# Kernel optimization log

Measured on AMD Instinct MI355X. Metric: run time of the kernel, lower is better.

The kernel has to match this reference:

```python
import jax, jax.numpy as jnp
import numpy as np

LSTM_SIZE = 32
NUM_OPS = 64
NUM_EDGE = 128
TEMPERATURE = 5.0
TANH_CONST = 2.5


def _lstm_cell(x, h, c, W_ih, W_hh, b_ih, b_hh):
    # PyTorch gate order: i, f, g, o
    g = x @ W_ih.T + b_ih + h @ W_hh.T + b_hh  # [4*H]
    i, f, gg, o = jnp.split(g, 4)
    c2 = jax.nn.sigmoid(f) * c + jax.nn.sigmoid(i) * jnp.tanh(gg)
    h2 = jax.nn.sigmoid(o) * jnp.tanh(c2)
    return h2, c2


def setup_inputs() -> dict:
    key = jax.random.key(0)
    ks = jax.random.split(key, 12)
    H, G, O = LSTM_SIZE, 4 * LSTM_SIZE, NUM_OPS
    s = 0.1
    return {
        "input_vars": jax.random.uniform(ks[0], (1, 1, H), jnp.float32, -s, s),
        "W_ih0": jax.random.uniform(ks[1], (G, H), jnp.float32, -s, s),
        "W_hh0": jax.random.uniform(ks[2], (G, H), jnp.float32, -s, s),
        "b_ih0": jax.random.uniform(ks[3], (G,), jnp.float32, -s, s),
        "b_hh0": jax.random.uniform(ks[4], (G,), jnp.float32, -s, s),
        "W_ih1": jax.random.uniform(ks[5], (G, H), jnp.float32, -s, s),
        "W_hh1": jax.random.uniform(ks[6], (G, H), jnp.float32, -s, s),
        "b_ih1": jax.random.uniform(ks[7], (G,), jnp.float32, -s, s),
        "b_hh1": jax.random.uniform(ks[8], (G,), jnp.float32, -s, s),
        "embd": jax.random.uniform(ks[9], (O, H), jnp.float32, -s, s),
        "W_pred": jax.random.uniform(ks[10], (O, H), jnp.float32, -s, s),
        "b_pred": jax.random.uniform(ks[11], (O,), jnp.float32, -s, s),
        "num_edge": NUM_EDGE,
    }


def reference(input_vars, W_ih0, W_hh0, b_ih0, b_hh0,
              W_ih1, W_hh1, b_ih1, b_hh1,
              embd, W_pred, b_pred, num_edge):
    H = input_vars.shape[-1]
    x0 = input_vars.reshape(H)
    z = jnp.zeros((H,), input_vars.dtype)
    key0 = jax.random.key(42)

    def step(carry, _):
        key, x, h0, c0, h1, c1 = carry
        h0, c0 = _lstm_cell(x, h0, c0, W_ih0, W_hh0, b_ih0, b_hh0)
        h1, c1 = _lstm_cell(h0, h1, c1, W_ih1, W_hh1, b_ih1, b_hh1)
        logits = TANH_CONST * jnp.tanh((h1 @ W_pred.T + b_pred) / TEMPERATURE)
        key, sub = jax.random.split(key)
        idx = jax.random.categorical(sub, logits)
        logp = jax.nn.log_softmax(logits)
        lp = logp[idx]
        ent = -jnp.sum(jnp.exp(logp) * logp)
        x = embd[idx]
        return (key, x, h0, c0, h1, c1), (lp, ent, idx)

    _, (lps, ents, arch) = jax.lax.scan(step, (key0, x0, z, z, z, z), None, length=num_edge)
    return jnp.sum(lps), jnp.sum(ents), arch
```

## Files before the change

kernel.cpp:

```cpp
#include <hip/hip_runtime.h>
#include <stdint.h>

namespace {

typedef float v2f __attribute__((ext_vector_type(2)));
typedef int   v2i __attribute__((ext_vector_type(2)));

constexpr int H      = 32;
constexpr int NEDGE  = 128;
constexpr float TINY   = 1.1754943508222875e-38f;
constexpr float L2E    = 1.4426950408889634f;
constexpr float LN2    = 0.6931471805599453f;

__device__ __forceinline__ void tf_round(uint32_t& x0, uint32_t& x1, int r) {
  x0 += x1;
  x1 = (x1 << r) | (x1 >> (32 - r));
  x1 ^= x0;
}

__device__ __forceinline__ void tf2x32(uint32_t k0, uint32_t k1,
                                       uint32_t& x0, uint32_t& x1) {
  const uint32_t ks2 = k0 ^ k1 ^ 0x1BD11BDAu;
  x0 += k0; x1 += k1;
  tf_round(x0,x1,13); tf_round(x0,x1,15); tf_round(x0,x1,26); tf_round(x0,x1, 6);
  x0 += k1;  x1 += ks2 + 1u;
  tf_round(x0,x1,17); tf_round(x0,x1,29); tf_round(x0,x1,16); tf_round(x0,x1,24);
  x0 += ks2; x1 += k0 + 2u;
  tf_round(x0,x1,13); tf_round(x0,x1,15); tf_round(x0,x1,26); tf_round(x0,x1, 6);
  x0 += k0;  x1 += k1 + 3u;
  tf_round(x0,x1,17); tf_round(x0,x1,29); tf_round(x0,x1,16); tf_round(x0,x1,24);
  x0 += k1;  x1 += ks2 + 4u;
  tf_round(x0,x1,13); tf_round(x0,x1,15); tf_round(x0,x1,26); tf_round(x0,x1, 6);
  x0 += ks2; x1 += k0 + 5u;
}

__device__ __forceinline__ float fexp(float x) {
  return __builtin_amdgcn_exp2f(x * L2E);
}
__device__ __forceinline__ float flog(float x) {
  return __builtin_amdgcn_logf(x) * LN2;
}
__device__ __forceinline__ float fsigmoid(float x) {
  return __builtin_amdgcn_rcpf(1.0f + __builtin_amdgcn_exp2f(-x * L2E));
}
__device__ __forceinline__ float ftanh(float x) {
  const float ax = __builtin_fabsf(x);
  const float t  = __builtin_amdgcn_exp2f(ax * (-2.0f * L2E));
  const float r  = (1.0f - t) * __builtin_amdgcn_rcpf(1.0f + t);
  return __builtin_copysignf(r, x);
}

__device__ __forceinline__ float rdlane(float v, int i) {
  return __int_as_float(__builtin_amdgcn_readlane(__float_as_int(v), i));
}

template <int CTRL>
__device__ __forceinline__ float dppf(float v) {
  return __int_as_float(__builtin_amdgcn_update_dpp(
      __float_as_int(v), __float_as_int(v), CTRL, 0xF, 0xF, false));
}

__device__ __forceinline__ float wave_sum64(float v) {
  v += dppf<0xB1>(v);
  v += dppf<0x4E>(v);
  v += dppf<0x141>(v);
  v += dppf<0x140>(v);
  return (rdlane(v, 15) + rdlane(v, 31)) + (rdlane(v, 47) + rdlane(v, 63));
}

__device__ __forceinline__ float wave_max64(float v) {
  v = fmaxf(v, dppf<0xB1>(v));
  v = fmaxf(v, dppf<0x4E>(v));
  v = fmaxf(v, dppf<0x141>(v));
  v = fmaxf(v, dppf<0x140>(v));
  return fmaxf(fmaxf(rdlane(v, 15), rdlane(v, 31)),
               fmaxf(rdlane(v, 47), rdlane(v, 63)));
}

__device__ __forceinline__ v2f pkfma(v2f a, v2f b, v2f c) {
  return __builtin_elementwise_fma(a, b, c);
}

__device__ __forceinline__ v2f permswap_pair(float g) {
  const v2i r = __builtin_amdgcn_permlane32_swap(
      __float_as_int(g), __float_as_int(g), false, false);
  return v2f{__int_as_float(r.x), __int_as_float(r.y)};
}

__global__ __launch_bounds__(192, 1)
void ctrl_kernel(const float* __restrict__ input_vars,
                 const float* __restrict__ W_ih0, const float* __restrict__ W_hh0,
                 const float* __restrict__ b_ih0, const float* __restrict__ b_hh0,
                 const float* __restrict__ W_ih1, const float* __restrict__ W_hh1,
                 const float* __restrict__ b_ih1, const float* __restrict__ b_hh1,
                 const float* __restrict__ embd,
                 const float* __restrict__ W_pred, const float* __restrict__ b_pred,
                 float* __restrict__ out) {
  const int tid  = threadIdx.x;
  const int lane = tid & 63;
  const int wid  = tid >> 6;
  const int rB   = lane + 64;

  __shared__ float4 Wh[2][8][128];
  __shared__ __align__(16) float embd_lds[65 * H];
  __shared__ __align__(16) float gumL[NEDGE][64];
  __shared__ __align__(16) float logitL[NEDGE][64];
  __shared__ __align__(16) float archL[NEDGE];
  __shared__ int gumflag;
  __shared__ int smflag;

  if (tid == 0) { gumflag = 0; smflag = 0; }

  if (wid < 2) {
#define STAGE(MAT, SRC)                                                    \
  _Pragma("unroll")                                                        \
  for (int j = 0; j < 8; ++j) {                                            \
    const int i = (tid & 127) + 128 * j;                                   \
    const int k4 = i & 7, row = i >> 3;                                    \
    Wh[MAT][k4][row] = reinterpret_cast<const float4*>(SRC)[row * 8 + k4]; \
  }
    STAGE(0, W_hh0)
    STAGE(1, W_hh1)
#undef STAGE
  } else {
#pragma unroll
    for (int j = 0; j < 8; ++j)
      reinterpret_cast<float4*>(embd_lds)[lane + 64 * j] =
          reinterpret_cast<const float4*>(embd)[lane + 64 * j];
    if (lane < 8)
      reinterpret_cast<float4*>(&embd_lds[64 * H])[lane] =
          reinterpret_cast<const float4*>(input_vars)[lane];
  }
  __syncthreads();
  if (wid == 1) return;

  if (wid == 2) {
    uint32_t k0 = 0u, k1 = 42u;
    for (int t = 0; t < NEDGE; ++t) {
      uint32_t r0 = 0u, r1 = (uint32_t)(lane & 1);
      tf2x32(k0, k1, r0, r1);
      const uint32_t n0 = (uint32_t)__builtin_amdgcn_readlane((int)r0, 0);
      const uint32_t n1 = (uint32_t)__builtin_amdgcn_readlane((int)r1, 0);
      const uint32_t s0 = (uint32_t)__builtin_amdgcn_readlane((int)r0, 1);
      const uint32_t s1 = (uint32_t)__builtin_amdgcn_readlane((int)r1, 1);
      uint32_t x0 = 0u, x1 = (uint32_t)lane;
      tf2x32(s0, s1, x0, x1);
      const uint32_t bits = x0 ^ x1;
      k0 = n0; k1 = n1;
      float u = __uint_as_float(0x3f800000u | (bits >> 9)) - 1.0f;
      u = fmaxf(u + TINY, TINY);
      gumL[t][lane] = -flog(-flog(u));
      __threadfence_block();
      *(volatile int*)&gumflag = t + 1;
    }
    float lp_sum = 0.f, ent_sum = 0.f;
    int seen = 0;
    for (int t = 0; t < NEDGE; ++t) {
      if (seen < t + 1) {
        int v = *(volatile int*)&smflag;
        while (v < t + 1) { __builtin_amdgcn_s_sleep(2); v = *(volatile int*)&smflag; }
        seen = v;
        __threadfence_block();
      }
      const float lg  = logitL[t][lane];
      const int  idxp = (int)archL[t];
      const float e  = fexp(lg);
      const float E  = wave_sum64(e);
      const float ES = wave_sum64(e * lg);
      const float lse = flog(E);
      const float li  = logitL[t][idxp];
      lp_sum  += li - lse;
      ent_sum += lse - ES / E;
    }
    if (lane == 0) { out[0] = lp_sum; out[1] = ent_sum; }
    return;
  }

  float4 wxA0[8], wxB0[8];
  float4 wx1A[8], wx1B[8];
  float4 wp4[8];
#pragma unroll
  for (int q = 0; q < 8; ++q) {
    wxA0[q] = reinterpret_cast<const float4*>(W_ih0 + lane * H)[q];
    wxB0[q] = reinterpret_cast<const float4*>(W_ih0 + rB * H)[q];
    wx1A[q] = reinterpret_cast<const float4*>(W_ih1 + lane * H)[q];
    wx1B[q] = reinterpret_cast<const float4*>(W_ih1 + rB * H)[q];
    wp4[q]  = reinterpret_cast<const float4*>(W_pred + lane * H)[q];
  }
  const float bsum0A = b_ih0[lane] + b_hh0[lane];
  const float bsum0B = b_ih0[rB]   + b_hh0[rB];
  const float bsum1A = b_ih1[lane] + b_hh1[lane];
  const float bsum1B = b_ih1[rB]   + b_hh1[rB];
  const float bp = b_pred[lane];

  float c0 = 0.f, h0v = 0.f, c1 = 0.f, h1v = 0.f;
  v2f hoA01={0.f,0.f}, hoA23={0.f,0.f}, hoB01={0.f,0.f}, hoB23={0.f,0.f};
  v2f r1A01={0.f,0.f}, r1A23={0.f,0.f}, r1B01={0.f,0.f}, r1B23={0.f,0.f};
  float xdA, xdB;
  {
    v2f xA01={0.f,0.f}, xA23={0.f,0.f}, xB01={0.f,0.f}, xB23={0.f,0.f};
#pragma unroll
    for (int q = 0; q < 8; ++q) {
      const float4 x4 = *reinterpret_cast<const float4*>(&embd_lds[64 * H + 4 * q]);
      xA01 = pkfma(v2f{x4.x, x4.y}, v2f{wxA0[q].x, wxA0[q].y}, xA01);
      xA23 = pkfma(v2f{x4.z, x4.w}, v2f{wxA0[q].z, wxA0[q].w}, xA23);
      xB01 = pkfma(v2f{x4.x, x4.y}, v2f{wxB0[q].x, wxB0[q].y}, xB01);
      xB23 = pkfma(v2f{x4.z, x4.w}, v2f{wxB0[q].z, wxB0[q].w}, xB23);
    }
    xdA = (xA01.x + xA01.y) + (xA23.x + xA23.y);
    xdB = (xB01.x + xB01.y) + (xB23.x + xB23.y);
  }

  int gseen = 0;
  for (int t = 0; t < NEDGE; ++t) {
    if (gseen < t + 1) {
      int v = *(volatile int*)&gumflag;
      while (v < t + 1) { __builtin_amdgcn_s_sleep(2); v = *(volatile int*)&gumflag; }
      gseen = v;
      __threadfence_block();
    }
    const float gum = gumL[t][lane];

    {
      const float gA = (bsum0A + xdA)
                     + ((hoA01.x + hoA01.y) + (hoA23.x + hoA23.y));
      const float gB = (bsum0B + xdB)
                     + ((hoB01.x + hoB01.y) + (hoB23.x + hoB23.y));
      const v2f gif = permswap_pair(gA);
      const v2f ggo = permswap_pair(gB);
      c0 = fsigmoid(gif.y) * c0 + fsigmoid(gif.x) * ftanh(ggo.x);
      h0v = fsigmoid(ggo.y) * ftanh(c0);
    }

    {
#pragma unroll
      for (int q = 0; q < 8; ++q) {
        const v2f h01 = {rdlane(h0v, 4*q+0), rdlane(h0v, 4*q+1)};
        const v2f h23 = {rdlane(h0v, 4*q+2), rdlane(h0v, 4*q+3)};
        r1A01 = pkfma(h01, v2f{wx1A[q].x, wx1A[q].y}, r1A01);
        r1A23 = pkfma(h23, v2f{wx1A[q].z, wx1A[q].w}, r1A23);
        r1B01 = pkfma(h01, v2f{wx1B[q].x, wx1B[q].y}, r1B01);
        r1B23 = pkfma(h23, v2f{wx1B[q].z, wx1B[q].w}, r1B23);
      }
      const float gA1 = bsum1A + ((r1A01.x + r1A01.y) + (r1A23.x + r1A23.y));
      const float gB1 = bsum1B + ((r1B01.x + r1B01.y) + (r1B23.x + r1B23.y));
      const v2f gif1 = permswap_pair(gA1);
      const v2f ggo1 = permswap_pair(gB1);
      c1  = fsigmoid(gif1.y) * c1 + fsigmoid(gif1.x) * ftanh(ggo1.x);
      h1v = fsigmoid(ggo1.y) * ftanh(c1);
    }

    v2f p01 = {0.f, 0.f}, p23 = {0.f, 0.f};
#pragma unroll
    for (int q = 0; q < 8; ++q) {
      const float4 w = wp4[q];
      p01 = pkfma(v2f{rdlane(h1v, 4*q+0), rdlane(h1v, 4*q+1)},
                  v2f{w.x, w.y}, p01);
      p23 = pkfma(v2f{rdlane(h1v, 4*q+2), rdlane(h1v, 4*q+3)},
                  v2f{w.z, w.w}, p23);
    }
    const float pre   = bp + ((p01.x + p01.y) + (p23.x + p23.y));
    const float logit = 2.5f * ftanh(pre * 0.2f);
    const float pert  = logit + gum;

    const float M = wave_max64(pert);
    const unsigned long long msk = __ballot(pert == M);
    const int idxu = __ffsll((long long)msk) - 1;

    archL[t] = (float)idxu;
    logitL[t][lane] = logit;
    __threadfence_block();
    *(volatile int*)&smflag = t + 1;

    {
      v2f xA01={0.f,0.f}, xA23={0.f,0.f}, xB01={0.f,0.f}, xB23={0.f,0.f};
#pragma unroll
      for (int q = 0; q < 8; ++q) {
        const float4 x4 =
            *reinterpret_cast<const float4*>(&embd_lds[idxu * H + 4 * q]);
        xA01 = pkfma(v2f{x4.x, x4.y}, v2f{wxA0[q].x, wxA0[q].y}, xA01);
        xA23 = pkfma(v2f{x4.z, x4.w}, v2f{wxA0[q].z, wxA0[q].w}, xA23);
        xB01 = pkfma(v2f{x4.x, x4.y}, v2f{wxB0[q].x, wxB0[q].y}, xB01);
        xB23 = pkfma(v2f{x4.z, x4.w}, v2f{wxB0[q].z, wxB0[q].w}, xB23);
      }
      xdA = (xA01.x + xA01.y) + (xA23.x + xA23.y);
      xdB = (xB01.x + xB01.y) + (xB23.x + xB23.y);

      hoA01 = v2f{0.f,0.f}; hoA23 = v2f{0.f,0.f};
      hoB01 = v2f{0.f,0.f}; hoB23 = v2f{0.f,0.f};
      r1A01 = v2f{0.f,0.f}; r1A23 = v2f{0.f,0.f};
      r1B01 = v2f{0.f,0.f}; r1B23 = v2f{0.f,0.f};
#pragma unroll
      for (int q = 0; q < 8; ++q) {
        const float4 wA = Wh[0][q][lane];
        const float4 wB = Wh[0][q][rB];
        const v2f h01 = {rdlane(h0v, 4*q+0), rdlane(h0v, 4*q+1)};
        const v2f h23 = {rdlane(h0v, 4*q+2), rdlane(h0v, 4*q+3)};
        hoA01 = pkfma(h01, v2f{wA.x, wA.y}, hoA01);
        hoA23 = pkfma(h23, v2f{wA.z, wA.w}, hoA23);
        hoB01 = pkfma(h01, v2f{wB.x, wB.y}, hoB01);
        hoB23 = pkfma(h23, v2f{wB.z, wB.w}, hoB23);
      }
#pragma unroll
      for (int q = 0; q < 8; ++q) {
        const float4 wA = Wh[1][q][lane];
        const float4 wB = Wh[1][q][rB];
        const v2f h01 = {rdlane(h1v, 4*q+0), rdlane(h1v, 4*q+1)};
        const v2f h23 = {rdlane(h1v, 4*q+2), rdlane(h1v, 4*q+3)};
        r1A01 = pkfma(h01, v2f{wA.x, wA.y}, r1A01);
        r1A23 = pkfma(h23, v2f{wA.z, wA.w}, r1A23);
        r1B01 = pkfma(h01, v2f{wB.x, wB.y}, r1B01);
        r1B23 = pkfma(h23, v2f{wB.z, wB.w}, r1B23);
      }
    }
  }

  out[2 + lane]      = archL[lane];
  out[2 + 64 + lane] = archL[64 + lane];
}

}

extern "C" void kernel_launch(void* const* d_in, const int* in_sizes, int n_in,
                              void* d_out, int out_size, void* d_ws, size_t ws_size,
                              hipStream_t stream) {
  (void)in_sizes; (void)n_in; (void)d_ws; (void)ws_size; (void)out_size;
  const float* input_vars = (const float*)d_in[0];
  const float* W_ih0 = (const float*)d_in[1];
  const float* W_hh0 = (const float*)d_in[2];
  const float* b_ih0 = (const float*)d_in[3];
  const float* b_hh0 = (const float*)d_in[4];
  const float* W_ih1 = (const float*)d_in[5];
  const float* W_hh1 = (const float*)d_in[6];
  const float* b_ih1 = (const float*)d_in[7];
  const float* b_hh1 = (const float*)d_in[8];
  const float* embd  = (const float*)d_in[9];
  const float* W_pred = (const float*)d_in[10];
  const float* b_pred = (const float*)d_in[11];
  float* out = (float*)d_out;

  hipLaunchKernelGGL(ctrl_kernel, dim3(1), dim3(192), 0, stream,
                     input_vars, W_ih0, W_hh0, b_ih0, b_hh0,
                     W_ih1, W_hh1, b_ih1, b_hh1,
                     embd, W_pred, b_pred, out);
}
```

Measured before the change: 147.1 us.

## Split LSTM layers across two waves with LDS flag handoff

Layer 0 now runs on wave 0 and layer 1 plus the prediction head and sampling on wave 1, where wave 1 previously exited early. The waves hand off h0 through a double-buffered LDS array and the sampled index through a progress flag. Wave 1 computes its recurrent product W_hh1·h1 before waiting for h0, which overlaps that work with layer 0's gate math. The cost is spin-wait synchronisation on the critical path every step, since layer 0 at step t+1 needs the index sampled at step t.

```diff
diff --git a/kernel.cpp b/kernel.cpp
--- a/kernel.cpp
+++ b/kernel.cpp
@@ -106,10 +106,12 @@
   __shared__ __align__(16) float gumL[NEDGE][64];
   __shared__ __align__(16) float logitL[NEDGE][64];
   __shared__ __align__(16) float archL[NEDGE];
+  __shared__ __align__(16) float h0bufD[2][H];
+  __shared__ int h0flag;
+  __shared__ int w1prog;
   __shared__ int gumflag;
-  __shared__ int smflag;
-
-  if (tid == 0) { gumflag = 0; smflag = 0; }
+
+  if (tid == 0) { h0flag = 0; w1prog = 0; gumflag = 0; }
 
   if (wid < 2) {
 #define STAGE(MAT, SRC)                                                    \
@@ -132,7 +134,6 @@
           reinterpret_cast<const float4*>(input_vars)[lane];
   }
   __syncthreads();
-  if (wid == 1) return;
 
   if (wid == 2) {
     uint32_t k0 = 0u, k1 = 42u;
@@ -154,14 +155,9 @@
       *(volatile int*)&gumflag = t + 1;
     }
     float lp_sum = 0.f, ent_sum = 0.f;
-    int seen = 0;
     for (int t = 0; t < NEDGE; ++t) {
-      if (seen < t + 1) {
-        int v = *(volatile int*)&smflag;
-        while (v < t + 1) { __builtin_amdgcn_s_sleep(2); v = *(volatile int*)&smflag; }
-        seen = v;
-        __threadfence_block();
-      }
+      while (*(volatile int*)&w1prog < t + 1) { __builtin_amdgcn_s_sleep(1); }
+      __threadfence_block();
       const float lg  = logitL[t][lane];
       const int  idxp = (int)archL[t];
       const float e  = fexp(lg);
@@ -176,52 +172,35 @@
     return;
   }
 
-  float4 wxA0[8], wxB0[8];
-  float4 wx1A[8], wx1B[8];
-  float4 wp4[8];
-#pragma unroll
-  for (int q = 0; q < 8; ++q) {
-    wxA0[q] = reinterpret_cast<const float4*>(W_ih0 + lane * H)[q];
-    wxB0[q] = reinterpret_cast<const float4*>(W_ih0 + rB * H)[q];
-    wx1A[q] = reinterpret_cast<const float4*>(W_ih1 + lane * H)[q];
-    wx1B[q] = reinterpret_cast<const float4*>(W_ih1 + rB * H)[q];
-    wp4[q]  = reinterpret_cast<const float4*>(W_pred + lane * H)[q];
-  }
-  const float bsum0A = b_ih0[lane] + b_hh0[lane];
-  const float bsum0B = b_ih0[rB]   + b_hh0[rB];
-  const float bsum1A = b_ih1[lane] + b_hh1[lane];
-  const float bsum1B = b_ih1[rB]   + b_hh1[rB];
-  const float bp = b_pred[lane];
-
-  float c0 = 0.f, h0v = 0.f, c1 = 0.f, h1v = 0.f;
-  v2f hoA01={0.f,0.f}, hoA23={0.f,0.f}, hoB01={0.f,0.f}, hoB23={0.f,0.f};
-  v2f r1A01={0.f,0.f}, r1A23={0.f,0.f}, r1B01={0.f,0.f}, r1B23={0.f,0.f};
-  float xdA, xdB;
-  {
-    v2f xA01={0.f,0.f}, xA23={0.f,0.f}, xB01={0.f,0.f}, xB23={0.f,0.f};
+  if (wid == 0) {
+    float4 wxA0[8], wxB0[8];
 #pragma unroll
     for (int q = 0; q < 8; ++q) {
-      const float4 x4 = *reinterpret_cast<const float4*>(&embd_lds[64 * H + 4 * q]);
-      xA01 = pkfma(v2f{x4.x, x4.y}, v2f{wxA0[q].x, wxA0[q].y}, xA01);
-      xA23 = pkfma(v2f{x4.z, x4.w}, v2f{wxA0[q].z, wxA0[q].w}, xA23);
-      xB01 = pkfma(v2f{x4.x, x4.y}, v2f{wxB0[q].x, wxB0[q].y}, xB01);
-      xB23 = pkfma(v2f{x4.z, x4.w}, v2f{wxB0[q].z, wxB0[q].w}, xB23);
-    }
-    xdA = (xA01.x + xA01.y) + (xA23.x + xA23.y);
-    xdB = (xB01.x + xB01.y) + (xB23.x + xB23.y);
-  }
-
-  int gseen = 0;
-  for (int t = 0; t < NEDGE; ++t) {
-    if (gseen < t + 1) {
-      int v = *(volatile int*)&gumflag;
-      while (v < t + 1) { __builtin_amdgcn_s_sleep(2); v = *(volatile int*)&gumflag; }
-      gseen = v;
-      __threadfence_block();
-    }
-    const float gum = gumL[t][lane];
-
+      wxA0[q] = reinterpret_cast<const float4*>(W_ih0 + lane * H)[q];
+      wxB0[q] = reinterpret_cast<const float4*>(W_ih0 + rB * H)[q];
+    }
+    const float bsum0A = b_ih0[lane] + b_hh0[lane];
+    const float bsum0B = b_ih0[rB]   + b_hh0[rB];
+
+    float c0 = 0.f, h0v = 0.f;
+    v2f hoA01={0.f,0.f}, hoA23={0.f,0.f}, hoB01={0.f,0.f}, hoB23={0.f,0.f};
+    float xdA, xdB;
     {
+      v2f xA01={0.f,0.f}, xA23={0.f,0.f}, xB01={0.f,0.f}, xB23={0.f,0.f};
+#pragma unroll
+      for (int q = 0; q < 8; ++q) {
+        const float4 x4 =
+            *reinterpret_cast<const float4*>(&embd_lds[64 * H + 4 * q]);
+        xA01 = pkfma(v2f{x4.x, x4.y}, v2f{wxA0[q].x, wxA0[q].y}, xA01);
+        xA23 = pkfma(v2f{x4.z, x4.w}, v2f{wxA0[q].z, wxA0[q].w}, xA23);
+        xB01 = pkfma(v2f{x4.x, x4.y}, v2f{wxB0[q].x, wxB0[q].y}, xB01);
+        xB23 = pkfma(v2f{x4.z, x4.w}, v2f{wxB0[q].z, wxB0[q].w}, xB23);
+      }
+      xdA = (xA01.x + xA01.y) + (xA23.x + xA23.y);
+      xdB = (xB01.x + xB01.y) + (xB23.x + xB23.y);
+    }
+
+    for (int t = 0; t < NEDGE; ++t) {
       const float gA = (bsum0A + xdA)
                      + ((hoA01.x + hoA01.y) + (hoA23.x + hoA23.y));
       const float gB = (bsum0B + xdB)
@@ -230,66 +209,12 @@
       const v2f ggo = permswap_pair(gB);
       c0 = fsigmoid(gif.y) * c0 + fsigmoid(gif.x) * ftanh(ggo.x);
       h0v = fsigmoid(ggo.y) * ftanh(c0);
-    }
-
-    {
-#pragma unroll
-      for (int q = 0; q < 8; ++q) {
-        const v2f h01 = {rdlane(h0v, 4*q+0), rdlane(h0v, 4*q+1)};
-        const v2f h23 = {rdlane(h0v, 4*q+2), rdlane(h0v, 4*q+3)};
-        r1A01 = pkfma(h01, v2f{wx1A[q].x, wx1A[q].y}, r1A01);
-        r1A23 = pkfma(h23, v2f{wx1A[q].z, wx1A[q].w}, r1A23);
-        r1B01 = pkfma(h01, v2f{wx1B[q].x, wx1B[q].y}, r1B01);
-        r1B23 = pkfma(h23, v2f{wx1B[q].z, wx1B[q].w}, r1B23);
-      }
-      const float gA1 = bsum1A + ((r1A01.x + r1A01.y) + (r1A23.x + r1A23.y));
-      const float gB1 = bsum1B + ((r1B01.x + r1B01.y) + (r1B23.x + r1B23.y));
-      const v2f gif1 = permswap_pair(gA1);
-      const v2f ggo1 = permswap_pair(gB1);
-      c1  = fsigmoid(gif1.y) * c1 + fsigmoid(gif1.x) * ftanh(ggo1.x);
-      h1v = fsigmoid(ggo1.y) * ftanh(c1);
-    }
-
-    v2f p01 = {0.f, 0.f}, p23 = {0.f, 0.f};
-#pragma unroll
-    for (int q = 0; q < 8; ++q) {
-      const float4 w = wp4[q];
-      p01 = pkfma(v2f{rdlane(h1v, 4*q+0), rdlane(h1v, 4*q+1)},
-                  v2f{w.x, w.y}, p01);
-      p23 = pkfma(v2f{rdlane(h1v, 4*q+2), rdlane(h1v, 4*q+3)},
-                  v2f{w.z, w.w}, p23);
-    }
-    const float pre   = bp + ((p01.x + p01.y) + (p23.x + p23.y));
-    const float logit = 2.5f * ftanh(pre * 0.2f);
-    const float pert  = logit + gum;
-
-    const float M = wave_max64(pert);
-    const unsigned long long msk = __ballot(pert == M);
-    const int idxu = __ffsll((long long)msk) - 1;
-
-    archL[t] = (float)idxu;
-    logitL[t][lane] = logit;
-    __threadfence_block();
-    *(volatile int*)&smflag = t + 1;
-
-    {
-      v2f xA01={0.f,0.f}, xA23={0.f,0.f}, xB01={0.f,0.f}, xB23={0.f,0.f};
-#pragma unroll
-      for (int q = 0; q < 8; ++q) {
-        const float4 x4 =
-            *reinterpret_cast<const float4*>(&embd_lds[idxu * H + 4 * q]);
-        xA01 = pkfma(v2f{x4.x, x4.y}, v2f{wxA0[q].x, wxA0[q].y}, xA01);
-        xA23 = pkfma(v2f{x4.z, x4.w}, v2f{wxA0[q].z, wxA0[q].w}, xA23);
-        xB01 = pkfma(v2f{x4.x, x4.y}, v2f{wxB0[q].x, wxB0[q].y}, xB01);
-        xB23 = pkfma(v2f{x4.z, x4.w}, v2f{wxB0[q].z, wxB0[q].w}, xB23);
-      }
-      xdA = (xA01.x + xA01.y) + (xA23.x + xA23.y);
-      xdB = (xB01.x + xB01.y) + (xB23.x + xB23.y);
+      h0bufD[t & 1][lane & 31] = h0v;
+      __threadfence_block();
+      *(volatile int*)&h0flag = t + 1;
 
       hoA01 = v2f{0.f,0.f}; hoA23 = v2f{0.f,0.f};
       hoB01 = v2f{0.f,0.f}; hoB23 = v2f{0.f,0.f};
-      r1A01 = v2f{0.f,0.f}; r1A23 = v2f{0.f,0.f};
-      r1B01 = v2f{0.f,0.f}; r1B23 = v2f{0.f,0.f};
 #pragma unroll
       for (int q = 0; q < 8; ++q) {
         const float4 wA = Wh[0][q][lane];
@@ -301,22 +226,105 @@
         hoB01 = pkfma(h01, v2f{wB.x, wB.y}, hoB01);
         hoB23 = pkfma(h23, v2f{wB.z, wB.w}, hoB23);
       }
+
+      if (t < NEDGE - 1) {
+        while (*(volatile int*)&w1prog < t + 1) {}
+        __threadfence_block();
+        const int idxu = (int)archL[t];
+        v2f xA01={0.f,0.f}, xA23={0.f,0.f}, xB01={0.f,0.f}, xB23={0.f,0.f};
+#pragma unroll
+        for (int q = 0; q < 8; ++q) {
+          const float4 x4 =
+              *reinterpret_cast<const float4*>(&embd_lds[idxu * H + 4 * q]);
+          xA01 = pkfma(v2f{x4.x, x4.y}, v2f{wxA0[q].x, wxA0[q].y}, xA01);
+          xA23 = pkfma(v2f{x4.z, x4.w}, v2f{wxA0[q].z, wxA0[q].w}, xA23);
+          xB01 = pkfma(v2f{x4.x, x4.y}, v2f{wxB0[q].x, wxB0[q].y}, xB01);
+          xB23 = pkfma(v2f{x4.z, x4.w}, v2f{wxB0[q].z, wxB0[q].w}, xB23);
+        }
+        xdA = (xA01.x + xA01.y) + (xA23.x + xA23.y);
+        xdB = (xB01.x + xB01.y) + (xB23.x + xB23.y);
+      }
+    }
+    return;
+  }
+
+  {
+    float4 wx1A[8], wx1B[8], wp4[8];
+#pragma unroll
+    for (int q = 0; q < 8; ++q) {
+      wx1A[q] = reinterpret_cast<const float4*>(W_ih1 + lane * H)[q];
+      wx1B[q] = reinterpret_cast<const float4*>(W_ih1 + rB * H)[q];
+      wp4[q]  = reinterpret_cast<const float4*>(W_pred + lane * H)[q];
+    }
+    const float bsum1A = b_ih1[lane] + b_hh1[lane];
+    const float bsum1B = b_ih1[rB]   + b_hh1[rB];
+    const float bp = b_pred[lane];
+
+    float c1 = 0.f, h1v = 0.f;
+
+    for (int t = 0; t < NEDGE; ++t) {
+      v2f rA01={0.f,0.f}, rA23={0.f,0.f}, rB01={0.f,0.f}, rB23={0.f,0.f};
 #pragma unroll
       for (int q = 0; q < 8; ++q) {
         const float4 wA = Wh[1][q][lane];
         const float4 wB = Wh[1][q][rB];
         const v2f h01 = {rdlane(h1v, 4*q+0), rdlane(h1v, 4*q+1)};
         const v2f h23 = {rdlane(h1v, 4*q+2), rdlane(h1v, 4*q+3)};
-        r1A01 = pkfma(h01, v2f{wA.x, wA.y}, r1A01);
-        r1A23 = pkfma(h23, v2f{wA.z, wA.w}, r1A23);
-        r1B01 = pkfma(h01, v2f{wB.x, wB.y}, r1B01);
-        r1B23 = pkfma(h23, v2f{wB.z, wB.w}, r1B23);
-      }
-    }
-  }
-
-  out[2 + lane]      = archL[lane];
-  out[2 + 64 + lane] = archL[64 + lane];
+        rA01 = pkfma(h01, v2f{wA.x, wA.y}, rA01);
+        rA23 = pkfma(h23, v2f{wA.z, wA.w}, rA23);
+        rB01 = pkfma(h01, v2f{wB.x, wB.y}, rB01);
+        rB23 = pkfma(h23, v2f{wB.z, wB.w}, rB23);
+      }
+
+      while (*(volatile int*)&gumflag < t + 1) {}
+      __threadfence_block();
+      const float gum = gumL[t][lane];
+
+      while (*(volatile int*)&h0flag < t + 1) {}
+      __threadfence_block();
+
+#pragma unroll
+      for (int q = 0; q < 8; ++q) {
+        const float4 h4 =
+            *reinterpret_cast<const float4*>(&h0bufD[t & 1][4 * q]);
+        rA01 = pkfma(v2f{h4.x, h4.y}, v2f{wx1A[q].x, wx1A[q].y}, rA01);
+        rA23 = pkfma(v2f{h4.z, h4.w}, v2f{wx1A[q].z, wx1A[q].w}, rA23);
+        rB01 = pkfma(v2f{h4.x, h4.y}, v2f{wx1B[q].x, wx1B[q].y}, rB01);
+        rB23 = pkfma(v2f{h4.z, h4.w}, v2f{wx1B[q].z, wx1B[q].w}, rB23);
+      }
+      const float gA1 = bsum1A + ((rA01.x + rA01.y) + (rA23.x + rA23.y));
+      const float gB1 = bsum1B + ((rB01.x + rB01.y) + (rB23.x + rB23.y));
+      const v2f gif1 = permswap_pair(gA1);
+      const v2f ggo1 = permswap_pair(gB1);
+      c1  = fsigmoid(gif1.y) * c1 + fsigmoid(gif1.x) * ftanh(ggo1.x);
+      h1v = fsigmoid(ggo1.y) * ftanh(c1);
+
+      v2f p01 = {0.f, 0.f}, p23 = {0.f, 0.f};
+#pragma unroll
+      for (int q = 0; q < 8; ++q) {
+        const float4 w = wp4[q];
+        p01 = pkfma(v2f{rdlane(h1v, 4*q+0), rdlane(h1v, 4*q+1)},
+                    v2f{w.x, w.y}, p01);
+        p23 = pkfma(v2f{rdlane(h1v, 4*q+2), rdlane(h1v, 4*q+3)},
+                    v2f{w.z, w.w}, p23);
+      }
+      const float pre   = bp + ((p01.x + p01.y) + (p23.x + p23.y));
+      const float logit = 2.5f * ftanh(pre * 0.2f);
+      const float pert  = logit + gum;
+
+      const float M = wave_max64(pert);
+      const unsigned long long msk = __ballot(pert == M);
+      const int idxu = __ffsll((long long)msk) - 1;
+
+      archL[t] = (float)idxu;
+      logitL[t][lane] = logit;
+      __threadfence_block();
+      *(volatile int*)&w1prog = t + 1;
+    }
+
+    out[2 + lane]      = archL[lane];
+    out[2 + 64 + lane] = archL[64 + lane];
+  }
 }
 
 }
```

Result: no change. 148.4 us (+0.9%).
